# Kernel tuning notes

Hardware: AMD Instinct MI355X
Metric: run time of the kernel (lower is better)

## Reference

```python
import jax, jax.numpy as jnp
import numpy as np
import math

PATCH = 32
NBINS = 36
EPS = 1e-18
PI = math.pi


def _sobel_grads(patch):
    # kornia SpatialGradient('sobel', 1, normalized=True): cross-correlation with
    # sobel kernels divided by sum(|k|)=8, replicate padding. out: [B,2,H,W]
    kx = jnp.array([[-1., 0., 1.], [-2., 0., 2.], [-1., 0., 1.]], dtype=patch.dtype) / 8.0
    ky = kx.T
    k = jnp.stack([kx, ky])[:, None]  # [2,1,3,3] OIHW
    p = jnp.pad(patch, ((0, 0), (0, 0), (1, 1), (1, 1)), mode='edge')
    return jax.lax.conv_general_dilated(p, k, (1, 1), 'VALID',
                                        dimension_numbers=('NCHW', 'OIHW', 'NCHW'))


def setup_inputs() -> dict:
    key = jax.random.key(0)
    B = 32768
    patch = jax.random.normal(key, (B, 1, PATCH, PATCH), dtype=jnp.float32)
    # default conf: gauss_weighted=False, circular_kernel=False -> ones kernel
    weight_kernel = jnp.ones((PATCH, PATCH), dtype=jnp.float32)
    # hard-coded circular Conv1d smoothing weights
    smooth_w = jnp.array([0.33, 0.34, 0.33], dtype=jnp.float32)
    return {"patch": patch, "weight_kernel": weight_kernel, "smooth_w": smooth_w}


def reference(patch, weight_kernel, smooth_w):
    B = patch.shape[0]
    HW = PATCH * PATCH
    g = _sobel_grads(patch) * weight_kernel          # [B,2,32,32]
    gx, gy = g[:, 0], g[:, 1]
    mag = jnp.sqrt(gx * gx + gy * gy + EPS)
    ori = jnp.arctan2(gy, gx + EPS) + 2.0 * PI
    # soft binning: linear split of magnitude between two adjacent angular bins
    o_big = NBINS * (ori + PI) / (2.0 * PI)
    bo0f = jnp.floor(o_big)
    w1 = o_big - bo0f
    bo0 = jnp.mod(bo0f, NBINS).astype(jnp.int32)
    bo1 = jnp.mod(bo0 + 1, NBINS)
    wo0 = (1.0 - w1) * mag
    wo1 = w1 * mag
    # fused scatter-histogram (replaces the 36-iteration mask+avg_pool loop);
    # adaptive_avg_pool2d(...,(1,1)) == mean over HW == scatter-sum / HW
    base = (jnp.arange(B, dtype=jnp.int32) * NBINS)[:, None]   # [B,1]
    ids = jnp.concatenate([(base + bo0.reshape(B, HW)).reshape(-1),
                           (base + bo1.reshape(B, HW)).reshape(-1)])
    vals = jnp.concatenate([wo0.reshape(-1), wo1.reshape(-1)])
    hist = jax.ops.segment_sum(vals, ids, num_segments=B * NBINS).reshape(B, NBINS) / HW
    # circular conv1d, kernel size 3, padding 1: out[i] = w0*h[i-1] + w1*h[i] + w2*h[i+1]
    hist_s = (smooth_w[0] * jnp.roll(hist, 1, axis=1)
              + smooth_w[1] * hist
              + smooth_w[2] * jnp.roll(hist, -1, axis=1))
    values = jnp.max(hist_s, axis=1)                 # [B]
    indices = jnp.argmax(hist_s, axis=1)             # [B]
    ip1 = jnp.mod(indices + 1, NBINS)
    im1 = jnp.mod(indices - 1, NBINS)
    vp1 = jnp.take_along_axis(hist_s, ip1[:, None], axis=1)[:, 0]
    vm1 = jnp.take_along_axis(hist_s, im1[:, None], axis=1)[:, 0]
    # parabolic sub-bin refinement (conf['ref']=False branch)
    refinement = (vp1 - vm1) / 2.0 / (2.0 * values - (vp1 + vm1))
    idx_ref = indices.astype(patch.dtype) + refinement
    angle = -(2.0 * PI * idx_ref / float(NBINS) - PI)  # conf['refined']=True
    return angle
```

## Files before the change

### kernel.cpp

```cpp
#include <hip/hip_runtime.h>
#include <math.h>

#define PATCH   32
#define NBINS   36
#define WPB     4
#define HW_N    (PATCH*PATCH)
#define TR      34
#define TC      35


__global__ __launch_bounds__(256, 2) void patch_dom_orient_kernel(
    const float* __restrict__ patch,
    const float* __restrict__ wk,
    const float* __restrict__ sw,
    float* __restrict__ out,
    int num_patches)
{
    __shared__ double tile[WPB][TR][TC];
    __shared__ double wkl[HW_N];
    __shared__ double hist[WPB][2][NBINS];
    __shared__ double hsm [WPB][NBINS];
    __shared__ double ctab[37];
    __shared__ double stab[37];

    const int tid  = threadIdx.x;
    const int w    = tid >> 6;
    const int lane = tid & 63;
    const int p    = blockIdx.x * WPB + w;
    const int pc   = (p < num_patches) ? p : (num_patches - 1);

    {
        double* hf = &hist[w][0][0];
        hf[lane] = 0.0;
        if (lane < 8) hf[64 + lane] = 0.0;
    }
    if (tid < 37) {
        double a = ((double)tid - 18.0) * 0.17453292519943295;
        ctab[tid] = cos(a);
        stab[tid] = sin(a);
    }
    {
        float4 v = reinterpret_cast<const float4*>(wk)[tid];
        double* dst = &wkl[tid * 4];
        dst[0] = (double)v.x * 0.125;
        dst[1] = (double)v.y * 0.125;
        dst[2] = (double)v.z * 0.125;
        dst[3] = (double)v.w * 0.125;
    }
    const float4* pp4 = reinterpret_cast<const float4*>(patch + (size_t)pc * HW_N);
    #pragma unroll
    for (int i = 0; i < 4; ++i) {
        int idx4 = i * 64 + lane;
        float4 v = pp4[idx4];
        int flat = idx4 * 4;
        int row = flat >> 5;
        int col = flat & 31;
        double* dst = &tile[w][row + 1][col + 1];
        dst[0] = (double)v.x;
        dst[1] = (double)v.y;
        dst[2] = (double)v.z;
        dst[3] = (double)v.w;
    }
    {
        int r = (lane >> 1) + 1;
        if (lane & 1) tile[w][r][33] = tile[w][r][32];
        else          tile[w][r][0]  = tile[w][r][1];
    }
    if (lane < 34) tile[w][0][lane]  = tile[w][1][lane];
    if (lane < 34) tile[w][33][lane] = tile[w][32][lane];
    __syncthreads();

    #pragma unroll 2
    for (int i = 0; i < HW_N / 64; ++i) {
        int idx = i * 64 + lane;
        int y = idx >> 5, x = idx & 31;
        const double* c0 = &tile[w][y + 1][x + 1];

        double pmm = c0[-TC - 1], pm0 = c0[-TC], pmp = c0[-TC + 1];
        double p0m = c0[-1],                     p0p = c0[1];
        double ppm = c0[ TC - 1], pp0 = c0[ TC], ppp = c0[ TC + 1];
        double wf  = wkl[idx];

        double d1 = pmp - pmm, d2 = p0p - p0m, d3 = ppp - ppm;
        double gx = (fma(d2, 2.0, d1) + d3) * wf;
        double e1 = ppm - pmm, e2 = pp0 - pm0, e3 = ppp - pmp;
        double gy = (fma(e2, 2.0, e1) + e3) * wf;

        double xs = gx + 1e-18;
        double m2 = fma(gx, gx, fma(gy, gy, 1e-18));

        float  rf = rsqrtf((float)m2);
        double r0 = (double)rf;
        double tt = r0 * r0;
        double hm = m2 * 0.5;
        double r  = r0 * fma(-hm, tt, 1.5);
        double mag = m2 * r;

        float xf = (float)xs, yf = (float)gy;
        float ax = fabsf(xf), ay = fabsf(yf);
        float mn = fminf(ax, ay), mx = fmaxf(ax, ay);
        float rr = mn * __builtin_amdgcn_rcpf(mx);
        float s2 = rr * rr;
        float at = rr * fmaf(s2, fmaf(s2, 0.0792f, -0.2885f), 0.9954f);
        if (ay > ax)   at = 1.5707963f - at;
        if (xf < 0.0f) at = 3.1415927f - at;
        at = copysignf(at, yf);
        int n = (int)rintf(at * 5.7295780f);
        n = (n < -18) ? -18 : ((n > 18) ? 18 : n);

        double cn = ctab[n + 18];
        double sn = stab[n + 18];
        double yr = fma(gy, cn, -(xs * sn));
        double z  = yr * r;
        double u  = z * z;
        double dl = z * fma(u, fma(u, fma(u, fma(u, 35.0 / 1152.0, 5.0 / 112.0),
                                          3.0 / 40.0), 1.0 / 6.0), 1.0);
        double phi = fma(dl, 5.729577951308232, (double)n);
        double fl  = floor(phi);
        double w1  = phi - fl;

        int bh = 54 + (int)fl;
        int b0 = bh - ((bh >= 36) ? 36 : 0);
        b0 = (b0 < 0) ? 0 : ((b0 > 35) ? 35 : b0);
        int b1 = (b0 == 35) ? 0 : b0 + 1;

        double wo1 = w1 * mag;
        double wo0 = mag - wo1;
        int rep = lane & 1;
        atomicAdd(&hist[w][rep][b0], wo0);
        atomicAdd(&hist[w][rep][b1], wo1);
    }
    __syncthreads();

    double hs_val = -INFINITY;
    if (lane < NBINS) {
        int im1 = (lane == 0) ? NBINS - 1 : lane - 1;
        int ip1 = (lane == NBINS - 1) ? 0 : lane + 1;
        double hm = hist[w][0][im1]  + hist[w][1][im1];
        double h0 = hist[w][0][lane] + hist[w][1][lane];
        double hp = hist[w][0][ip1]  + hist[w][1][ip1];
        hs_val = ((double)sw[0] * hm + (double)sw[1] * h0 + (double)sw[2] * hp)
                 * (1.0 / 1024.0);
        hsm[w][lane] = hs_val;
    }
    __syncthreads();

    double v  = hs_val;
    int    bi = (lane < NBINS) ? lane : 64;
    #pragma unroll
    for (int sft = 32; sft > 0; sft >>= 1) {
        double ov = __shfl_xor(v, sft, 64);
        int    oi = __shfl_xor(bi, sft, 64);
        if (ov > v || (ov == v && oi < bi)) { v = ov; bi = oi; }
    }

    if (lane == 0 && p < num_patches) {
        int ip = (bi == NBINS - 1) ? 0 : bi + 1;
        int im = (bi == 0) ? NBINS - 1 : bi - 1;
        double vp1 = hsm[w][ip];
        double vm1 = hsm[w][im];
        double refinement = ((vp1 - vm1) / 2.0) / (2.0 * v - (vp1 + vm1));
        double idx_ref = (double)bi + refinement;
        double angle = -((2.0 * M_PI * idx_ref) / 36.0 - M_PI);
        out[p] = (float)angle;
    }
}

extern "C" void kernel_launch(void* const* d_in, const int* in_sizes, int n_in,
                              void* d_out, int out_size, void* d_ws, size_t ws_size,
                              hipStream_t stream) {
    const float* patch = (const float*)d_in[0];
    const float* wk    = (const float*)d_in[1];
    const float* sw    = (const float*)d_in[2];
    float* out = (float*)d_out;

    int num_patches = in_sizes[0] / HW_N;
    int blocks = (num_patches + WPB - 1) / WPB;

    patch_dom_orient_kernel<<<blocks, 256, 0, stream>>>(patch, wk, sw, out, num_patches);
}
```

Before: 274.5 us.

## Store patch tile as float, drop weight LDS copy, widen histogram replicas

The shared patch tile is stored in float instead of double with a 36-wide row, and the weight-kernel LDS copy is removed in favour of direct global loads. Together these cut LDS use enough to raise launch bounds to 4 blocks per CU. Histogram replicas go from 2 to 4 to reduce atomic contention, and the floor in binning is replaced by an int truncation after adding an offset of 54. Occupancy should rise, at the cost of per-pixel float-to-double conversions and global weight loads inside the loop.

```diff
diff --git a/kernel.cpp b/kernel.cpp
--- a/kernel.cpp
+++ b/kernel.cpp
@@ -6,19 +6,19 @@
 #define WPB     4
 #define HW_N    (PATCH*PATCH)
 #define TR      34
-#define TC      35
+#define TC      36
+#define NREP    4
 
 
-__global__ __launch_bounds__(256, 2) void patch_dom_orient_kernel(
+__global__ __launch_bounds__(256, 4) void patch_dom_orient_kernel(
     const float* __restrict__ patch,
     const float* __restrict__ wk,
     const float* __restrict__ sw,
     float* __restrict__ out,
     int num_patches)
 {
-    __shared__ double tile[WPB][TR][TC];
-    __shared__ double wkl[HW_N];
-    __shared__ double hist[WPB][2][NBINS];
+    __shared__ float  tile[WPB][TR][TC];
+    __shared__ double hist[WPB][NREP][NBINS];
     __shared__ double hsm [WPB][NBINS];
     __shared__ double ctab[37];
     __shared__ double stab[37];
@@ -32,20 +32,13 @@
     {
         double* hf = &hist[w][0][0];
         hf[lane] = 0.0;
-        if (lane < 8) hf[64 + lane] = 0.0;
+        hf[64 + lane] = 0.0;
+        if (lane < 16) hf[128 + lane] = 0.0;
     }
     if (tid < 37) {
         double a = ((double)tid - 18.0) * 0.17453292519943295;
         ctab[tid] = cos(a);
         stab[tid] = sin(a);
-    }
-    {
-        float4 v = reinterpret_cast<const float4*>(wk)[tid];
-        double* dst = &wkl[tid * 4];
-        dst[0] = (double)v.x * 0.125;
-        dst[1] = (double)v.y * 0.125;
-        dst[2] = (double)v.z * 0.125;
-        dst[3] = (double)v.w * 0.125;
     }
     const float4* pp4 = reinterpret_cast<const float4*>(patch + (size_t)pc * HW_N);
     #pragma unroll
@@ -55,11 +48,8 @@
         int flat = idx4 * 4;
         int row = flat >> 5;
         int col = flat & 31;
-        double* dst = &tile[w][row + 1][col + 1];
-        dst[0] = (double)v.x;
-        dst[1] = (double)v.y;
-        dst[2] = (double)v.z;
-        dst[3] = (double)v.w;
+        float* dst = &tile[w][row + 1][col + 1];
+        dst[0] = v.x; dst[1] = v.y; dst[2] = v.z; dst[3] = v.w;
     }
     {
         int r = (lane >> 1) + 1;
@@ -70,18 +60,19 @@
     if (lane < 34) tile[w][33][lane] = tile[w][32][lane];
     __syncthreads();
 
+    const float* tbase = &tile[w][0][0];
     #pragma unroll 2
     for (int i = 0; i < HW_N / 64; ++i) {
         int idx = i * 64 + lane;
-        int y = idx >> 5, x = idx & 31;
-        const double* c0 = &tile[w][y + 1][x + 1];
+        const float* c0 = tbase + idx + ((idx >> 5) << 2);
 
-        double pmm = c0[-TC - 1], pm0 = c0[-TC], pmp = c0[-TC + 1];
-        double p0m = c0[-1],                     p0p = c0[1];
-        double ppm = c0[ TC - 1], pp0 = c0[ TC], ppp = c0[ TC + 1];
-        double wf  = wkl[idx];
+        double pmm = (double)c0[0],      pm0 = (double)c0[1],      pmp = (double)c0[2];
+        double p0m = (double)c0[TC],                               p0p = (double)c0[TC + 2];
+        double ppm = (double)c0[2 * TC], pp0 = (double)c0[2 * TC + 1], ppp = (double)c0[2 * TC + 2];
+        double wf  = (double)wk[idx] * 0.125;
 
-        double d1 = pmp - pmm, d2 = p0p - p0m, d3 = ppp - ppm;
+        double d1 = pmp - pmm, d2 = p0p - p0m, d3 = ppp - pmp + (pmp - ppm);
+        d3 = ppp - ppm;
         double gx = (fma(d2, 2.0, d1) + d3) * wf;
         double e1 = ppm - pmm, e2 = pp0 - pm0, e3 = ppp - pmp;
         double gy = (fma(e2, 2.0, e1) + e3) * wf;
@@ -89,11 +80,8 @@
         double xs = gx + 1e-18;
         double m2 = fma(gx, gx, fma(gy, gy, 1e-18));
 
-        float  rf = rsqrtf((float)m2);
-        double r0 = (double)rf;
-        double tt = r0 * r0;
-        double hm = m2 * 0.5;
-        double r  = r0 * fma(-hm, tt, 1.5);
+        double r0 = (double)__builtin_amdgcn_rsqf((float)m2);
+        double r  = r0 * fma(-(m2 * 0.5), r0 * r0, 1.5);
         double mag = m2 * r;
 
         float xf = (float)xs, yf = (float)gy;
@@ -115,20 +103,18 @@
         double u  = z * z;
         double dl = z * fma(u, fma(u, fma(u, fma(u, 35.0 / 1152.0, 5.0 / 112.0),
                                           3.0 / 40.0), 1.0 / 6.0), 1.0);
-        double phi = fma(dl, 5.729577951308232, (double)n);
-        double fl  = floor(phi);
-        double w1  = phi - fl;
-
-        int bh = 54 + (int)fl;
+        double ph2 = fma(dl, 5.729577951308232, (double)(n + 54));
+        int bh = (int)ph2;
+        double w1 = ph2 - (double)bh;
         int b0 = bh - ((bh >= 36) ? 36 : 0);
         b0 = (b0 < 0) ? 0 : ((b0 > 35) ? 35 : b0);
         int b1 = (b0 == 35) ? 0 : b0 + 1;
 
         double wo1 = w1 * mag;
         double wo0 = mag - wo1;
-        int rep = lane & 1;
-        atomicAdd(&hist[w][rep][b0], wo0);
-        atomicAdd(&hist[w][rep][b1], wo1);
+        double* hrep = &hist[w][lane & (NREP - 1)][0];
+        atomicAdd(&hrep[b0], wo0);
+        atomicAdd(&hrep[b1], wo1);
     }
     __syncthreads();
 
@@ -136,9 +122,12 @@
     if (lane < NBINS) {
         int im1 = (lane == 0) ? NBINS - 1 : lane - 1;
         int ip1 = (lane == NBINS - 1) ? 0 : lane + 1;
-        double hm = hist[w][0][im1]  + hist[w][1][im1];
-        double h0 = hist[w][0][lane] + hist[w][1][lane];
-        double hp = hist[w][0][ip1]  + hist[w][1][ip1];
+        double hm = hist[w][0][im1]  + hist[w][1][im1]
+                  + hist[w][2][im1]  + hist[w][3][im1];
+        double h0 = hist[w][0][lane] + hist[w][1][lane]
+                  + hist[w][2][lane] + hist[w][3][lane];
+        double hp = hist[w][0][ip1]  + hist[w][1][ip1]
+                  + hist[w][2][ip1]  + hist[w][3][ip1];
         hs_val = ((double)sw[0] * hm + (double)sw[1] * h0 + (double)sw[2] * hp)
                  * (1.0 / 1024.0);
         hsm[w][lane] = hs_val;
```

New measurement: 256.2 us. 1.07x faster.
